# Kernel tuning notes

Hardware: AMD Instinct MI355X
Metric: run time of the kernel (lower is better)

The kernel has to match this reference:

```python
import jax, jax.numpy as jnp
import numpy as np

NL = 2    # num_layers
H = 4     # attention heads
C = 512   # hidden_dim
IN = 256  # in_dim
F = 16    # fanout
B = 256   # seed nodes
NC = 47   # num_classes
DH = C // H
EPS = 1e-5


def _ln(x, g, b):
    mu = jnp.mean(x, -1, keepdims=True)
    var = jnp.mean((x - mu) ** 2, -1, keepdims=True)
    return (x - mu) * jax.lax.rsqrt(var + EPS) * g + b


def _mha(x, wqkv, bqkv, wo, bo):
    # torch nn.MultiheadAttention with a single batch of N tokens
    n = x.shape[0]
    qkv = x @ wqkv.T + bqkv                      # [N, 3C]
    q, k, v = jnp.split(qkv, 3, axis=-1)
    q = q.reshape(n, H, DH).transpose(1, 0, 2)   # [H, N, DH]
    k = k.reshape(n, H, DH).transpose(1, 0, 2)
    v = v.reshape(n, H, DH).transpose(1, 0, 2)
    s = jnp.einsum('hnd,hmd->hnm', q, k) * (1.0 / float(np.sqrt(DH)))
    a = jax.nn.softmax(s, axis=-1)
    o = jnp.einsum('hnm,hmd->hnd', a, v).transpose(1, 0, 2).reshape(n, C)
    return o @ wo.T + bo


def setup_inputs() -> dict:
    ks = jax.random.split(jax.random.key(0), 16)
    n = [B, B * F, B * F * F]
    p = lambda i, shape: jax.random.normal(ks[i], shape, jnp.float32) * 0.02
    return {
        'feats0': jax.random.normal(ks[0], (n[0], IN), jnp.float32),
        'feats1': jax.random.normal(ks[1], (n[1], IN), jnp.float32),
        'feats2': jax.random.normal(ks[2], (n[2], IN), jnp.float32),
        'nmask0': jnp.ones((n[0],), jnp.float32),
        'nmask1': jnp.ones((n[1],), jnp.float32),
        'nmask2': jnp.ones((n[2],), jnp.float32),
        'nbmask0': jax.random.randint(ks[3], (n[0], F), 0, 2, jnp.int32),
        'nbmask1': jax.random.randint(ks[4], (n[1], F), 0, 2, jnp.int32),
        'emb_w': p(5, (C, IN)), 'emb_b': jnp.zeros((C,), jnp.float32),
        'sage_w': p(6, (NL, C, 2 * C)), 'sage_b': jnp.zeros((NL, C), jnp.float32),
        'qkv_w': p(7, (NL, 3 * C, C)), 'qkv_b': jnp.zeros((NL, 3 * C), jnp.float32),
        'out_w': p(8, (NL, C, C)), 'out_b': jnp.zeros((NL, C), jnp.float32),
        'n1_g': jnp.ones((NL, C), jnp.float32), 'n1_b': jnp.zeros((NL, C), jnp.float32),
        'n2_g': jnp.ones((NL, C), jnp.float32), 'n2_b': jnp.zeros((NL, C), jnp.float32),
        'ffn_w1': p(9, (NL, 2 * C, C)), 'ffn_b1': jnp.zeros((NL, 2 * C), jnp.float32),
        'ffn_w2': p(10, (NL, C, 2 * C)), 'ffn_b2': jnp.zeros((NL, C), jnp.float32),
        'cls_w': p(11, (NC, C)), 'cls_b': jnp.zeros((NC,), jnp.float32),
    }


def reference(feats0, feats1, feats2, nmask0, nmask1, nmask2, nbmask0, nbmask1,
              emb_w, emb_b, sage_w, sage_b, qkv_w, qkv_b, out_w, out_b,
              n1_g, n1_b, n2_g, n2_b, ffn_w1, ffn_b1, ffn_w2, ffn_b2, cls_w, cls_b):
    nmasks = [nmask0, nmask1, nmask2]
    nbm = [nbmask0.astype(jnp.float32), nbmask1.astype(jnp.float32)]
    # embedding + node-mask gating per depth
    states = [(f @ emb_w.T + emb_b) * m[:, None]
              for f, m in zip([feats0, feats1, feats2], nmasks)]
    for li in range(NL):
        prev = states
        nxt = list(prev)
        for depth in range(NL - li - 1, -1, -1):
            # masked mean aggregation of sampled neighbors: [n_d, F, C] -> [n_d, C]
            child = prev[depth + 1].reshape(-1, F, C)
            m = nbm[depth][:, :, None]
            summed = jnp.sum(child * m, axis=1)
            denom = jnp.clip(jnp.sum(m, axis=1), 1.0)
            agg = summed / denom
            sf = prev[depth]
            # GraphSAGE concat update (no activation, dropout=0)
            h_local = jnp.concatenate([sf, agg], -1) @ sage_w[li].T + sage_b[li]
            h = _ln(sf + h_local, n1_g[li], n1_b[li])
            h = _ln(h + _mha(h, qkv_w[li], qkv_b[li], out_w[li], out_b[li]),
                    n2_g[li], n2_b[li])
            hf = jax.nn.relu(h @ ffn_w1[li].T + ffn_b1[li]) @ ffn_w2[li].T + ffn_b2[li]
            nxt[depth] = (h + hf) * nmasks[depth][:, None]
        states = nxt
    return states[0] @ cls_w.T + cls_b
```

## Files before the change

kernel.cpp:

```cpp
#include <hip/hip_runtime.h>
#include <math.h>


typedef unsigned short bf16_t;
typedef __attribute__((ext_vector_type(8))) short bf16x8_t;
typedef __attribute__((ext_vector_type(4))) float f32x4_t;

__device__ __forceinline__ bf16_t f2bf(float f) {
  union { float f; unsigned u; } v; v.f = f;
  unsigned r = v.u + 0x7FFFu + ((v.u >> 16) & 1u);
  return (bf16_t)(r >> 16);
}
__device__ __forceinline__ float bf2f(bf16_t u) {
  union { unsigned u; float f; } v; v.u = ((unsigned)u) << 16; return v.f;
}
__device__ __forceinline__ unsigned cvtpk(float lo, float hi) {
  unsigned r;
  asm("v_cvt_pk_bf16_f32 %0, %1, %2" : "=v"(r) : "v"(lo), "v"(hi));
  return r;
}
__device__ __forceinline__ void gload16(const void* g, void* l) {
  __builtin_amdgcn_global_load_lds(
      (const __attribute__((address_space(1))) unsigned int*)g,
      (__attribute__((address_space(3))) unsigned int*)l, 16, 0, 0);
}

#define QSCALE (0.08838834764831845f * 1.4426950408889634f)

template <int BM, int BN, int MODE, bool SPLIT>
__global__ __launch_bounds__(256) void mgemm(
    const bf16_t* __restrict__ A, const bf16_t* __restrict__ A2,
    const bf16_t* __restrict__ W, const float* __restrict__ bias,
    const bf16_t* __restrict__ res, const float* __restrict__ rowa,
    const float* __restrict__ rowb, float* __restrict__ Cf,
    bf16_t* __restrict__ Cb, bf16_t* __restrict__ Vt,
    int M, int N, int K) {
  constexpr int FM = BM / 32, FN = BN / 32;
  constexpr int NCH = (BM + BN) / 16;
  constexpr int CPW = NCH / 4;
  __shared__ bf16_t lds[2][(BM + BN) * 32];
  const int t = threadIdx.x;
  const int w = t >> 6, lane = t & 63;
  const int g = lane >> 4, li = lane & 15;
  const int bm = blockIdx.x * BM, bn = blockIdx.y * BN;
  const int wr = (w >> 1) * (BM / 2), wc = (w & 1) * (BN / 2);
  f32x4_t acc[FM][FN] = {};

  auto stage = [&](int buf, int k0) {
#pragma unroll
    for (int c0 = 0; c0 < CPW; ++c0) {
      const int c = w * CPW + c0;
      const int row = c * 16 + (lane >> 2);
      const int gk = k0 + (lane & 3) * 8;
      const bf16_t* src;
      if (row < BM) {
        if (SPLIT) {
          src = (gk < 512) ? (A + (size_t)(bm + row) * 512 + gk)
                           : (A2 + (size_t)(bm + row) * 512 + (gk - 512));
        } else {
          src = A + (size_t)(bm + row) * K + gk;
        }
      } else {
        src = W + (size_t)(bn + row - BM) * K + gk;
      }
      gload16(src, &lds[buf][c * 512]);
    }
  };

  const int nk = K / 32;
  stage(0, 0);
  for (int ks = 0; ks < nk; ++ks) {
    __syncthreads();
    if (ks + 1 < nk) stage((ks + 1) & 1, (ks + 1) * 32);
    const bf16_t* As = &lds[ks & 1][0];
    const bf16_t* Bs = &lds[ks & 1][BM * 32];
    bf16x8_t af[FM], bfr[FN];
#pragma unroll
    for (int i = 0; i < FM; ++i)
      af[i] = *(const bf16x8_t*)(As + (wr + i * 16 + li) * 32 + g * 8);
#pragma unroll
    for (int j = 0; j < FN; ++j)
      bfr[j] = *(const bf16x8_t*)(Bs + (wc + j * 16 + li) * 32 + g * 8);
#pragma unroll
    for (int i = 0; i < FM; ++i)
#pragma unroll
      for (int j = 0; j < FN; ++j)
        acc[i][j] = __builtin_amdgcn_mfma_f32_16x16x32_bf16(
            af[i], bfr[j], acc[i][j], 0, 0, 0);
  }

#pragma unroll
  for (int i = 0; i < FM; ++i) {
    const int mb = bm + wr + i * 16 + g * 4;
#pragma unroll
    for (int j = 0; j < FN; ++j) {
      const int n = bn + wc + j * 16 + li;
      if (MODE == 5) {
        const float bb = bias[n];
        if (n < 512) {
#pragma unroll
          for (int r = 0; r < 4; ++r)
            Cb[(size_t)(mb + r) * 1024 + n] = f2bf((acc[i][j][r] + bb) * QSCALE);
        } else if (n < 1024) {
#pragma unroll
          for (int r = 0; r < 4; ++r)
            Cb[(size_t)(mb + r) * 1024 + n] = f2bf(acc[i][j][r] + bb);
        } else {
          ushort4 o;
          o.x = f2bf(acc[i][j][0] + bb); o.y = f2bf(acc[i][j][1] + bb);
          o.z = f2bf(acc[i][j][2] + bb); o.w = f2bf(acc[i][j][3] + bb);
          *(ushort4*)(Vt + (size_t)(n - 1024) * M + mb) = o;
        }
      } else {
#pragma unroll
        for (int r = 0; r < 4; ++r) {
          const int m = mb + r;
          const float v = acc[i][j][r];
          if (MODE == 0) Cf[(size_t)m * N + n] = v + bias[n];
          if (MODE == 1) Cb[(size_t)m * N + n] = f2bf((v + bias[n]) * rowa[m]);
          if (MODE == 2)
            Cb[(size_t)m * N + n] = f2bf((v + bias[n] * rowa[m]) * rowb[m]);
          if (MODE == 3) Cb[(size_t)m * N + n] = f2bf(fmaxf(v + bias[n], 0.f));
          if (MODE == 4)
            Cb[(size_t)m * N + n] =
                f2bf((v + bias[n] + bf2f(res[(size_t)m * N + n])) * rowa[m]);
        }
      }
    }
  }
}

template <int SPLITS>
__global__ __launch_bounds__(256) void flashT(
    const bf16_t* __restrict__ qk, const bf16_t* __restrict__ vt,
    bf16_t* __restrict__ attno, float* __restrict__ Of,
    float* __restrict__ Ml, int N) {
  __shared__ bf16_t Ks[2][64 * 128];
  __shared__ bf16_t Vs[2][128 * 64];
  __shared__ bf16_t Ps[4][16 * 64];
  const int bid = blockIdx.x;
  const int sp = bid % SPLITS;
  const int h = (bid / SPLITS) & 3;
  const int qb = bid / (4 * SPLITS);
  const int t = threadIdx.x, w = t >> 6, lane = t & 63;
  const int g = lane >> 4, li = lane & 15;
  const int kvbase = sp * (N / SPLITS);
  const int nt = (N / SPLITS) >> 6;

  bf16x8_t qf[4];
  {
    const bf16_t* qrow = qk + (size_t)(qb * 64 + w * 16 + li) * 1024 + h * 128;
#pragma unroll
    for (int ks = 0; ks < 4; ++ks)
      qf[ks] = *(const bf16x8_t*)(qrow + ks * 32 + g * 8);
  }

  int koff[4], voff[2], pwoff[4];
#pragma unroll
  for (int ks = 0; ks < 4; ++ks)
    koff[ks] = li * 256 + (((ks * 4 + g) ^ (li & 7)) << 4);
#pragma unroll
  for (int ks = 0; ks < 2; ++ks)
    voff[ks] = li * 128 + (((ks * 4 + g) ^ (li & 7)) << 4);
#pragma unroll
  for (int mf = 0; mf < 4; ++mf)
    pwoff[mf] = li * 128 + (((mf * 2 + (g >> 1)) ^ (li & 7)) << 4) +
                ((g & 1) << 3);
  char* Pb = (char*)Ps + w * 2048;

  const bf16_t* kp[4];
  const bf16_t* vp[4];
#pragma unroll
  for (int i = 0; i < 4; ++i) {
    const int c = w * 4 + i;
    const int rk = c * 4 + (lane >> 4);
    kp[i] = qk + (size_t)(kvbase + rk) * 1024 + 512 + h * 128 +
            (((lane & 15) ^ (rk & 7)) * 8);
    const int rv = c * 8 + (lane >> 3);
    vp[i] = vt + (size_t)(h * 128 + rv) * N + kvbase +
            (((lane & 7) ^ (rv & 7)) * 8);
  }
  auto stage = [&](int buf) {
#pragma unroll
    for (int i = 0; i < 4; ++i) {
      const int c = w * 4 + i;
      gload16(kp[i], &Ks[buf][c * 512]);
      kp[i] += 64 * 1024;
      gload16(vp[i], &Vs[buf][c * 512]);
      vp[i] += 64;
    }
  };

  f32x4_t acc[8] = {};
  float mrun = -1e30f, lrun = 0.f;
  stage(0);
  for (int tt = 0; tt < nt; ++tt) {
    const int cur = tt & 1;
    __syncthreads();
    if (tt + 1 < nt) stage(cur ^ 1);
    const char* Kb = (const char*)Ks + cur * 16384;
    const char* Vb = (const char*)Vs + cur * 16384;

    f32x4_t sf[4] = {};
    __builtin_amdgcn_s_setprio(1);
#pragma unroll
    for (int ks = 0; ks < 4; ++ks) {
#pragma unroll
      for (int mf = 0; mf < 4; ++mf) {
        const bf16x8_t kf = *(const bf16x8_t*)(Kb + koff[ks] + mf * 4096);
        sf[mf] =
            __builtin_amdgcn_mfma_f32_16x16x32_bf16(kf, qf[ks], sf[mf], 0, 0, 0);
      }
    }
    __builtin_amdgcn_s_setprio(0);

    float tmax = -1e30f;
#pragma unroll
    for (int mf = 0; mf < 4; ++mf)
#pragma unroll
      for (int r = 0; r < 4; ++r) tmax = fmaxf(tmax, sf[mf][r]);
    tmax = fmaxf(tmax, __shfl_xor(tmax, 16));
    tmax = fmaxf(tmax, __shfl_xor(tmax, 32));
    if (!__all(tmax - mrun <= 11.0f)) {
      const float mnew = fmaxf(mrun, tmax);
      const float fsc = exp2f(mrun - mnew);
      mrun = mnew;
      lrun *= fsc;
#pragma unroll
      for (int mf = 0; mf < 8; ++mf) acc[mf] *= fsc;
    }
    float lsum = 0.f;
#pragma unroll
    for (int mf = 0; mf < 4; ++mf)
#pragma unroll
      for (int r = 0; r < 4; ++r) {
        const float p = exp2f(sf[mf][r] - mrun);
        sf[mf][r] = p;
        lsum += p;
      }
    lsum += __shfl_xor(lsum, 16);
    lsum += __shfl_xor(lsum, 32);
    lrun += lsum;

#pragma unroll
    for (int mf = 0; mf < 4; ++mf) {
      uint2 pv;
      pv.x = cvtpk(sf[mf][0], sf[mf][1]);
      pv.y = cvtpk(sf[mf][2], sf[mf][3]);
      *(uint2*)(Pb + pwoff[mf]) = pv;
    }
    __builtin_amdgcn_s_setprio(1);
#pragma unroll
    for (int ks = 0; ks < 2; ++ks) {
      const bf16x8_t pf = *(const bf16x8_t*)(Pb + voff[ks]);
#pragma unroll
      for (int mf = 0; mf < 8; ++mf) {
        const bf16x8_t vf = *(const bf16x8_t*)(Vb + voff[ks] + mf * 2048);
        acc[mf] =
            __builtin_amdgcn_mfma_f32_16x16x32_bf16(vf, pf, acc[mf], 0, 0, 0);
      }
    }
    __builtin_amdgcn_s_setprio(0);
  }

  if (SPLITS == 1) {
    const float invl = 1.f / lrun;
#pragma unroll
    for (int mf = 0; mf < 8; ++mf) {
      ushort4 o;
      o.x = f2bf(acc[mf][0] * invl); o.y = f2bf(acc[mf][1] * invl);
      o.z = f2bf(acc[mf][2] * invl); o.w = f2bf(acc[mf][3] * invl);
      *(ushort4*)(attno + (size_t)(qb * 64 + w * 16 + li) * 512 + h * 128 +
                  mf * 16 + g * 4) = o;
    }
  } else {
    const int q = qb * 64 + w * 16 + li;
#pragma unroll
    for (int mf = 0; mf < 8; ++mf)
      *(f32x4_t*)(Of + ((size_t)sp * N + q) * 512 + h * 128 + mf * 16 + g * 4) =
          acc[mf];
    if (lane < 16) {
      float2 ml; ml.x = mrun; ml.y = lrun;
      *(float2*)(Ml + ((size_t)(sp * 4 + h) * N + q) * 2) = ml;
    }
  }
}

template <int SPLITS>
__global__ __launch_bounds__(256) void merge_attn(
    const float* __restrict__ Of, const float* __restrict__ Ml,
    bf16_t* __restrict__ attno, int N) {
  const int q = blockIdx.x, t = threadIdx.x;
#pragma unroll
  for (int half = 0; half < 2; ++half) {
    const int c = t + half * 256;
    const int h = c >> 7;
    float2 ml[SPLITS];
    float m = -1e30f;
#pragma unroll
    for (int s = 0; s < SPLITS; ++s) {
      ml[s] = ((const float2*)Ml)[(s * 4 + h) * N + q];
      m = fmaxf(m, ml[s].x);
    }
    float num = 0.f, den = 0.f;
#pragma unroll
    for (int s = 0; s < SPLITS; ++s) {
      const float wgt = exp2f(ml[s].x - m);
      num += Of[((size_t)s * N + q) * 512 + c] * wgt;
      den += ml[s].y * wgt;
    }
    attno[(size_t)q * 512 + c] = f2bf(num / den);
  }
}

__global__ __launch_bounds__(256) void add_ln(
    const bf16_t* __restrict__ X, const float* __restrict__ Y,
    const float* __restrict__ gg, const float* __restrict__ bb,
    bf16_t* __restrict__ out) {
  const int row = blockIdx.x, t = threadIdx.x;
  const size_t base = (size_t)row * 512;
  const float x0 = bf2f(X[base + t]) + Y[base + t];
  const float x1 = bf2f(X[base + 256 + t]) + Y[base + 256 + t];
  float s = x0 + x1, ss = x0 * x0 + x1 * x1;
#pragma unroll
  for (int o = 32; o > 0; o >>= 1) {
    s += __shfl_down(s, o);
    ss += __shfl_down(ss, o);
  }
  __shared__ float rs[4], rss[4], sm[2];
  const int wv = t >> 6, ln = t & 63;
  if (ln == 0) { rs[wv] = s; rss[wv] = ss; }
  __syncthreads();
  if (t == 0) {
    const float S = rs[0] + rs[1] + rs[2] + rs[3];
    const float SS = rss[0] + rss[1] + rss[2] + rss[3];
    const float mean = S * (1.f / 512.f);
    sm[0] = mean;
    sm[1] = rsqrtf(SS * (1.f / 512.f) - mean * mean + 1e-5f);
  }
  __syncthreads();
  const float mean = sm[0], rstd = sm[1];
  out[base + t] = f2bf((x0 - mean) * rstd * gg[t] + bb[t]);
  out[base + 256 + t] = f2bf((x1 - mean) * rstd * gg[t + 256] + bb[t + 256]);
}

__global__ __launch_bounds__(256) void agg_feats(
    const float* __restrict__ feats2, const int* __restrict__ nbm,
    const float* __restrict__ nm2, bf16_t* __restrict__ aggF,
    float* __restrict__ sw, float* __restrict__ invd) {
  const int i = blockIdx.x, t = threadIdx.x;
  float acc = 0.f, ws = 0.f, nbs = 0.f;
#pragma unroll
  for (int j = 0; j < 16; ++j) {
    const float nb = (float)nbm[i * 16 + j];
    const float wj = nb * nm2[i * 16 + j];
    acc += wj * feats2[(size_t)(i * 16 + j) * 256 + t];
    ws += wj;
    nbs += nb;
  }
  aggF[(size_t)i * 256 + t] = f2bf(acc);
  if (t == 0) { sw[i] = ws; invd[i] = 1.f / fmaxf(nbs, 1.f); }
}

__global__ __launch_bounds__(256) void agg_state(
    const bf16_t* __restrict__ src, const int* __restrict__ nbm,
    bf16_t* __restrict__ agg) {
  const int i = blockIdx.x, t = threadIdx.x;
  float a0 = 0.f, a1 = 0.f, nbs = 0.f;
#pragma unroll
  for (int j = 0; j < 16; ++j) {
    const float nb = (float)nbm[i * 16 + j];
    const bf16_t* r = src + (size_t)(i * 16 + j) * 512;
    a0 += nb * bf2f(r[t]);
    a1 += nb * bf2f(r[t + 256]);
    nbs += nb;
  }
  const float inv = 1.f / fmaxf(nbs, 1.f);
  agg[(size_t)i * 512 + t] = f2bf(a0 * inv);
  agg[(size_t)i * 512 + 256 + t] = f2bf(a1 * inv);
}

__global__ __launch_bounds__(256) void cvt_all(
    const float* __restrict__ s_emb, const float* __restrict__ s_sage,
    const float* __restrict__ s_qkv, const float* __restrict__ s_out,
    const float* __restrict__ s_f1, const float* __restrict__ s_f2,
    const float* __restrict__ s_ft0, const float* __restrict__ s_ft1,
    bf16_t* __restrict__ d_emb, bf16_t* __restrict__ d_sage,
    bf16_t* __restrict__ d_qkv, bf16_t* __restrict__ d_out,
    bf16_t* __restrict__ d_f1, bf16_t* __restrict__ d_f2,
    bf16_t* __restrict__ d_ft0, bf16_t* __restrict__ d_ft1) {
  int i = blockIdx.x * 256 + threadIdx.x;
  const float* s; bf16_t* d; int base;
  if (i < 32768)        { s = s_emb;  d = d_emb;  base = 0; }
  else if (i < 294912)  { s = s_sage; d = d_sage; base = 32768; }
  else if (i < 688128)  { s = s_qkv;  d = d_qkv;  base = 294912; }
  else if (i < 819200)  { s = s_out;  d = d_out;  base = 688128; }
  else if (i < 1081344) { s = s_f1;   d = d_f1;   base = 819200; }
  else if (i < 1343488) { s = s_f2;   d = d_f2;   base = 1081344; }
  else if (i < 1359872) { s = s_ft0;  d = d_ft0;  base = 1343488; }
  else                  { s = s_ft1;  d = d_ft1;  base = 1359872; }
  i -= base;
  const float4 v = ((const float4*)s)[i];
  ushort4 o;
  o.x = f2bf(v.x); o.y = f2bf(v.y); o.z = f2bf(v.z); o.w = f2bf(v.w);
  ((ushort4*)d)[i] = o;
}

__global__ __launch_bounds__(256) void cls_k(
    const bf16_t* __restrict__ s, const float* __restrict__ wc,
    const float* __restrict__ bc, float* __restrict__ out) {
  __shared__ float srow[512];
  const int m = blockIdx.x, t = threadIdx.x;
  srow[t] = bf2f(s[(size_t)m * 512 + t]);
  srow[t + 256] = bf2f(s[(size_t)m * 512 + 256 + t]);
  __syncthreads();
  if (t < 47) {
    float a = bc[t];
    const float* wr = wc + (size_t)t * 512;
    for (int k = 0; k < 512; ++k) a += srow[k] * wr[k];
    out[(size_t)m * 47 + t] = a;
  }
}

struct LayerW {
  const bf16_t *wsage, *wqkv, *wout, *wf1, *wf2;
  const float *bsage, *bqkv, *bout, *bf1, *bf2;
  const float *n1g, *n1b, *n2g, *n2b;
};
struct Scratch {
  float* tmp;
  bf16_t *h1, *h2, *qkb, *vt, *attno, *f1o;
  float *Of, *Ml;
};

static void run_block(int n, const bf16_t* sf, const bf16_t* agg,
                      const float* nmask, const LayerW& L, const Scratch& S,
                      bf16_t* sout, hipStream_t st) {
  if (n == 4096) {
    mgemm<64, 128, 0, true><<<dim3(64, 4), 256, 0, st>>>(
        sf, agg, L.wsage, L.bsage, nullptr, nullptr, nullptr, S.tmp, nullptr,
        nullptr, n, 512, 1024);
  } else {
    mgemm<64, 64, 0, true><<<dim3(4, 8), 256, 0, st>>>(
        sf, agg, L.wsage, L.bsage, nullptr, nullptr, nullptr, S.tmp, nullptr,
        nullptr, n, 512, 1024);
  }
  add_ln<<<n, 256, 0, st>>>(sf, S.tmp, L.n1g, L.n1b, S.h1);
  if (n == 4096) {
    mgemm<128, 128, 5, false><<<dim3(32, 12), 256, 0, st>>>(
        S.h1, nullptr, L.wqkv, L.bqkv, nullptr, nullptr, nullptr, nullptr,
        S.qkb, S.vt, n, 1536, 512);
    flashT<2><<<(n / 64) * 8, 256, 0, st>>>(S.qkb, S.vt, nullptr, S.Of, S.Ml, n);
    merge_attn<2><<<n, 256, 0, st>>>(S.Of, S.Ml, S.attno, n);
    mgemm<64, 128, 0, false><<<dim3(64, 4), 256, 0, st>>>(
        S.attno, nullptr, L.wout, L.bout, nullptr, nullptr, nullptr, S.tmp,
        nullptr, nullptr, n, 512, 512);
  } else {
    mgemm<64, 64, 5, false><<<dim3(4, 24), 256, 0, st>>>(
        S.h1, nullptr, L.wqkv, L.bqkv, nullptr, nullptr, nullptr, nullptr,
        S.qkb, S.vt, n, 1536, 512);
    flashT<1><<<(n / 64) * 4, 256, 0, st>>>(S.qkb, S.vt, S.attno, nullptr,
                                            nullptr, n);
    mgemm<64, 64, 0, false><<<dim3(4, 8), 256, 0, st>>>(
        S.attno, nullptr, L.wout, L.bout, nullptr, nullptr, nullptr, S.tmp,
        nullptr, nullptr, n, 512, 512);
  }
  add_ln<<<n, 256, 0, st>>>(S.h1, S.tmp, L.n2g, L.n2b, S.h2);
  if (n == 4096) {
    mgemm<128, 128, 3, false><<<dim3(32, 8), 256, 0, st>>>(
        S.h2, nullptr, L.wf1, L.bf1, nullptr, nullptr, nullptr, nullptr, S.f1o,
        nullptr, n, 1024, 512);
    mgemm<64, 128, 4, false><<<dim3(64, 4), 256, 0, st>>>(
        S.f1o, nullptr, L.wf2, L.bf2, S.h2, nmask, nullptr, nullptr, sout,
        nullptr, n, 512, 1024);
  } else {
    mgemm<64, 64, 3, false><<<dim3(4, 16), 256, 0, st>>>(
        S.h2, nullptr, L.wf1, L.bf1, nullptr, nullptr, nullptr, nullptr, S.f1o,
        nullptr, n, 1024, 512);
    mgemm<64, 64, 4, false><<<dim3(4, 8), 256, 0, st>>>(
        S.f1o, nullptr, L.wf2, L.bf2, S.h2, nmask, nullptr, nullptr, sout,
        nullptr, n, 512, 1024);
  }
}

extern "C" void kernel_launch(void* const* d_in, const int* in_sizes, int n_in,
                              void* d_out, int out_size, void* d_ws,
                              size_t ws_size, hipStream_t stream) {
  const float* feats0 = (const float*)d_in[0];
  const float* feats1 = (const float*)d_in[1];
  const float* feats2 = (const float*)d_in[2];
  const float* nmask0 = (const float*)d_in[3];
  const float* nmask1 = (const float*)d_in[4];
  const float* nmask2 = (const float*)d_in[5];
  const int* nbmask0 = (const int*)d_in[6];
  const int* nbmask1 = (const int*)d_in[7];
  const float* emb_w = (const float*)d_in[8];
  const float* emb_b = (const float*)d_in[9];
  const float* sage_w = (const float*)d_in[10];
  const float* sage_b = (const float*)d_in[11];
  const float* qkv_w = (const float*)d_in[12];
  const float* qkv_b = (const float*)d_in[13];
  const float* out_w = (const float*)d_in[14];
  const float* out_b = (const float*)d_in[15];
  const float* n1_g = (const float*)d_in[16];
  const float* n1_b = (const float*)d_in[17];
  const float* n2_g = (const float*)d_in[18];
  const float* n2_b = (const float*)d_in[19];
  const float* ffn_w1 = (const float*)d_in[20];
  const float* ffn_b1 = (const float*)d_in[21];
  const float* ffn_w2 = (const float*)d_in[22];
  const float* ffn_b2 = (const float*)d_in[23];
  const float* cls_w = (const float*)d_in[24];
  const float* cls_b = (const float*)d_in[25];
  float* out = (float*)d_out;

  size_t off = 0;
  auto alloc = [&](size_t bytes) {
    void* r = (char*)d_ws + off;
    off += (bytes + 255) & ~(size_t)255;
    return r;
  };
  bf16_t* wemb = (bf16_t*)alloc((size_t)512 * 256 * 2);
  bf16_t* wsage = (bf16_t*)alloc((size_t)2 * 512 * 1024 * 2);
  bf16_t* wqkv = (bf16_t*)alloc((size_t)2 * 1536 * 512 * 2);
  bf16_t* wout = (bf16_t*)alloc((size_t)2 * 512 * 512 * 2);
  bf16_t* wf1 = (bf16_t*)alloc((size_t)2 * 1024 * 512 * 2);
  bf16_t* wf2 = (bf16_t*)alloc((size_t)2 * 512 * 1024 * 2);
  bf16_t* f0b = (bf16_t*)alloc((size_t)256 * 256 * 2);
  bf16_t* f1b = (bf16_t*)alloc((size_t)4096 * 256 * 2);
  bf16_t* s0 = (bf16_t*)alloc((size_t)256 * 512 * 2);
  bf16_t* s0b = (bf16_t*)alloc((size_t)256 * 512 * 2);
  bf16_t* s0f = (bf16_t*)alloc((size_t)256 * 512 * 2);
  bf16_t* s1 = (bf16_t*)alloc((size_t)4096 * 512 * 2);
  bf16_t* s1b = (bf16_t*)alloc((size_t)4096 * 512 * 2);
  bf16_t* aggFb = (bf16_t*)alloc((size_t)4096 * 256 * 2);
  float* swv = (float*)alloc((size_t)4096 * 4);
  float* invd = (float*)alloc((size_t)4096 * 4);
  bf16_t* aggb = (bf16_t*)alloc((size_t)4096 * 512 * 2);
  float* tmp = (float*)alloc((size_t)4096 * 512 * 4);
  bf16_t* h1 = (bf16_t*)alloc((size_t)4096 * 512 * 2);
  bf16_t* h2 = (bf16_t*)alloc((size_t)4096 * 512 * 2);
  bf16_t* qkb = (bf16_t*)alloc((size_t)4096 * 1024 * 2);
  bf16_t* vt = (bf16_t*)alloc((size_t)512 * 4096 * 2);
  bf16_t* attno = (bf16_t*)alloc((size_t)4096 * 512 * 2);
  bf16_t* f1o = (bf16_t*)alloc((size_t)4096 * 1024 * 2);
  float* Of = (float*)alloc((size_t)2 * 4096 * 512 * 4);
  float* Ml = (float*)alloc((size_t)2 * 4 * 4096 * 2 * 4);

  cvt_all<<<6336, 256, 0, stream>>>(emb_w, sage_w, qkv_w, out_w, ffn_w1,
                                    ffn_w2, feats0, feats1, wemb, wsage, wqkv,
                                    wout, wf1, wf2, f0b, f1b);

  mgemm<64, 128, 1, false><<<dim3(64, 4), 256, 0, stream>>>(
      f1b, nullptr, wemb, emb_b, nullptr, nmask1, nullptr, nullptr, s1, nullptr,
      4096, 512, 256);
  mgemm<64, 64, 1, false><<<dim3(4, 8), 256, 0, stream>>>(
      f0b, nullptr, wemb, emb_b, nullptr, nmask0, nullptr, nullptr, s0, nullptr,
      256, 512, 256);
  agg_feats<<<4096, 256, 0, stream>>>(feats2, nbmask1, nmask2, aggFb, swv, invd);
  mgemm<64, 128, 2, false><<<dim3(64, 4), 256, 0, stream>>>(
      aggFb, nullptr, wemb, emb_b, nullptr, swv, invd, nullptr, aggb, nullptr,
      4096, 512, 256);

  LayerW L0{wsage, wqkv, wout, wf1, wf2,
            sage_b, qkv_b, out_b, ffn_b1, ffn_b2,
            n1_g, n1_b, n2_g, n2_b};
  LayerW L1{wsage + 512 * 1024, wqkv + 1536 * 512, wout + 512 * 512,
            wf1 + 1024 * 512, wf2 + 512 * 1024,
            sage_b + 512, qkv_b + 1536, out_b + 512, ffn_b1 + 1024,
            ffn_b2 + 512, n1_g + 512, n1_b + 512, n2_g + 512, n2_b + 512};
  Scratch S{tmp, h1, h2, qkb, vt, attno, f1o, Of, Ml};

  run_block(4096, s1, aggb, nmask1, L0, S, s1b, stream);
  agg_state<<<256, 256, 0, stream>>>(s1, nbmask0, aggb);
  run_block(256, s0, aggb, nmask0, L0, S, s0b, stream);
  agg_state<<<256, 256, 0, stream>>>(s1b, nbmask0, aggb);
  run_block(256, s0b, aggb, nmask0, L1, S, s0f, stream);

  cls_k<<<256, 256, 0, stream>>>(s0f, cls_w, cls_b, out);
}
```

Measured before the change: 321.3 us.

## Use 128-row flash tiles with 4 KV splits and bf16 intermediates

The N=4096 attention now runs 128 query rows per block with 512 threads, which halves the K/V reloads per query. The KV sequence is split four ways to keep the grid large. Split partial outputs are normalized and stored as bf16 instead of fp32, and the merge reweights them using l*exp2(m). The GEMM MODE 0 output (the tmp buffer feeding add_ln) also becomes bf16, which cuts memory traffic. In exchange, rounding of intermediates to bf16 adds precision loss, and the extra split adds merge reads.

```diff
diff --git a/kernel.cpp b/kernel.cpp
--- a/kernel.cpp
+++ b/kernel.cpp
@@ -32,7 +32,7 @@
     const bf16_t* __restrict__ A, const bf16_t* __restrict__ A2,
     const bf16_t* __restrict__ W, const float* __restrict__ bias,
     const bf16_t* __restrict__ res, const float* __restrict__ rowa,
-    const float* __restrict__ rowb, float* __restrict__ Cf,
+    const float* __restrict__ rowb,
     bf16_t* __restrict__ Cb, bf16_t* __restrict__ Vt,
     int M, int N, int K) {
   constexpr int FM = BM / 32, FN = BN / 32;
@@ -116,7 +116,7 @@
         for (int r = 0; r < 4; ++r) {
           const int m = mb + r;
           const float v = acc[i][j][r];
-          if (MODE == 0) Cf[(size_t)m * N + n] = v + bias[n];
+          if (MODE == 0) Cb[(size_t)m * N + n] = f2bf(v + bias[n]);
           if (MODE == 1) Cb[(size_t)m * N + n] = f2bf((v + bias[n]) * rowa[m]);
           if (MODE == 2)
             Cb[(size_t)m * N + n] = f2bf((v + bias[n] * rowa[m]) * rowb[m]);
@@ -130,14 +130,16 @@
   }
 }
 
-template <int SPLITS>
-__global__ __launch_bounds__(256) void flashT(
+template <int QB, int SPLITS>
+__global__ __launch_bounds__(QB * 4) void flashT(
     const bf16_t* __restrict__ qk, const bf16_t* __restrict__ vt,
-    bf16_t* __restrict__ attno, float* __restrict__ Of,
+    bf16_t* __restrict__ attno, bf16_t* __restrict__ Ofb,
     float* __restrict__ Ml, int N) {
+  constexpr int NW = QB / 16;
+  constexpr int KCH = 16 / NW;
   __shared__ bf16_t Ks[2][64 * 128];
   __shared__ bf16_t Vs[2][128 * 64];
-  __shared__ bf16_t Ps[4][16 * 64];
+  __shared__ bf16_t Ps[NW][16 * 64];
   const int bid = blockIdx.x;
   const int sp = bid % SPLITS;
   const int h = (bid / SPLITS) & 3;
@@ -149,7 +151,7 @@
 
   bf16x8_t qf[4];
   {
-    const bf16_t* qrow = qk + (size_t)(qb * 64 + w * 16 + li) * 1024 + h * 128;
+    const bf16_t* qrow = qk + (size_t)(qb * QB + w * 16 + li) * 1024 + h * 128;
 #pragma unroll
     for (int ks = 0; ks < 4; ++ks)
       qf[ks] = *(const bf16x8_t*)(qrow + ks * 32 + g * 8);
@@ -168,11 +170,11 @@
                 ((g & 1) << 3);
   char* Pb = (char*)Ps + w * 2048;
 
-  const bf16_t* kp[4];
-  const bf16_t* vp[4];
-#pragma unroll
-  for (int i = 0; i < 4; ++i) {
-    const int c = w * 4 + i;
+  const bf16_t* kp[KCH];
+  const bf16_t* vp[KCH];
+#pragma unroll
+  for (int i = 0; i < KCH; ++i) {
+    const int c = w * KCH + i;
     const int rk = c * 4 + (lane >> 4);
     kp[i] = qk + (size_t)(kvbase + rk) * 1024 + 512 + h * 128 +
             (((lane & 15) ^ (rk & 7)) * 8);
@@ -182,8 +184,8 @@
   }
   auto stage = [&](int buf) {
 #pragma unroll
-    for (int i = 0; i < 4; ++i) {
-      const int c = w * 4 + i;
+    for (int i = 0; i < KCH; ++i) {
+      const int c = w * KCH + i;
       gload16(kp[i], &Ks[buf][c * 512]);
       kp[i] += 64 * 1024;
       gload16(vp[i], &Vs[buf][c * 512]);
@@ -263,22 +265,25 @@
     __builtin_amdgcn_s_setprio(0);
   }
 
+  const float invl = 1.f / lrun;
+  const int q = qb * QB + w * 16 + li;
   if (SPLITS == 1) {
-    const float invl = 1.f / lrun;
 #pragma unroll
     for (int mf = 0; mf < 8; ++mf) {
       ushort4 o;
       o.x = f2bf(acc[mf][0] * invl); o.y = f2bf(acc[mf][1] * invl);
       o.z = f2bf(acc[mf][2] * invl); o.w = f2bf(acc[mf][3] * invl);
-      *(ushort4*)(attno + (size_t)(qb * 64 + w * 16 + li) * 512 + h * 128 +
-                  mf * 16 + g * 4) = o;
+      *(ushort4*)(attno + (size_t)q * 512 + h * 128 + mf * 16 + g * 4) = o;
     }
   } else {
-    const int q = qb * 64 + w * 16 + li;
-#pragma unroll
-    for (int mf = 0; mf < 8; ++mf)
-      *(f32x4_t*)(Of + ((size_t)sp * N + q) * 512 + h * 128 + mf * 16 + g * 4) =
-          acc[mf];
+#pragma unroll
+    for (int mf = 0; mf < 8; ++mf) {
+      ushort4 o;
+      o.x = f2bf(acc[mf][0] * invl); o.y = f2bf(acc[mf][1] * invl);
+      o.z = f2bf(acc[mf][2] * invl); o.w = f2bf(acc[mf][3] * invl);
+      *(ushort4*)(Ofb + ((size_t)sp * N + q) * 512 + h * 128 + mf * 16 +
+                  g * 4) = o;
+    }
     if (lane < 16) {
       float2 ml; ml.x = mrun; ml.y = lrun;
       *(float2*)(Ml + ((size_t)(sp * 4 + h) * N + q) * 2) = ml;
@@ -288,7 +293,7 @@
 
 template <int SPLITS>
 __global__ __launch_bounds__(256) void merge_attn(
-    const float* __restrict__ Of, const float* __restrict__ Ml,
+    const bf16_t* __restrict__ Ofb, const float* __restrict__ Ml,
     bf16_t* __restrict__ attno, int N) {
   const int q = blockIdx.x, t = threadIdx.x;
 #pragma unroll
@@ -305,22 +310,22 @@
     float num = 0.f, den = 0.f;
 #pragma unroll
     for (int s = 0; s < SPLITS; ++s) {
-      const float wgt = exp2f(ml[s].x - m);
-      num += Of[((size_t)s * N + q) * 512 + c] * wgt;
-      den += ml[s].y * wgt;
+      const float wgt = ml[s].y * exp2f(ml[s].x - m);
+      num += bf2f(Ofb[((size_t)s * N + q) * 512 + c]) * wgt;
+      den += wgt;
     }
     attno[(size_t)q * 512 + c] = f2bf(num / den);
   }
 }
 
 __global__ __launch_bounds__(256) void add_ln(
-    const bf16_t* __restrict__ X, const float* __restrict__ Y,
+    const bf16_t* __restrict__ X, const bf16_t* __restrict__ Y,
     const float* __restrict__ gg, const float* __restrict__ bb,
     bf16_t* __restrict__ out) {
   const int row = blockIdx.x, t = threadIdx.x;
   const size_t base = (size_t)row * 512;
-  const float x0 = bf2f(X[base + t]) + Y[base + t];
-  const float x1 = bf2f(X[base + 256 + t]) + Y[base + 256 + t];
+  const float x0 = bf2f(X[base + t]) + bf2f(Y[base + t]);
+  const float x1 = bf2f(X[base + 256 + t]) + bf2f(Y[base + 256 + t]);
   float s = x0 + x1, ss = x0 * x0 + x1 * x1;
 #pragma unroll
   for (int o = 32; o > 0; o >>= 1) {
@@ -428,9 +433,8 @@
   const float *n1g, *n1b, *n2g, *n2b;
 };
 struct Scratch {
-  float* tmp;
-  bf16_t *h1, *h2, *qkb, *vt, *attno, *f1o;
-  float *Of, *Ml;
+  bf16_t *tmpb, *h1, *h2, *qkb, *vt, *attno, *f1o, *Ofb;
+  float *Ml;
 };
 
 static void run_block(int n, const bf16_t* sf, const bf16_t* agg,
@@ -438,48 +442,49 @@
                       bf16_t* sout, hipStream_t st) {
   if (n == 4096) {
     mgemm<64, 128, 0, true><<<dim3(64, 4), 256, 0, st>>>(
-        sf, agg, L.wsage, L.bsage, nullptr, nullptr, nullptr, S.tmp, nullptr,
-        nullptr, n, 512, 1024);
+        sf, agg, L.wsage, L.bsage, nullptr, nullptr, nullptr, S.tmpb, nullptr,
+        n, 512, 1024);
   } else {
     mgemm<64, 64, 0, true><<<dim3(4, 8), 256, 0, st>>>(
-        sf, agg, L.wsage, L.bsage, nullptr, nullptr, nullptr, S.tmp, nullptr,
-        nullptr, n, 512, 1024);
-  }
-  add_ln<<<n, 256, 0, st>>>(sf, S.tmp, L.n1g, L.n1b, S.h1);
+        sf, agg, L.wsage, L.bsage, nullptr, nullptr, nullptr, S.tmpb, nullptr,
+        n, 512, 1024);
+  }
+  add_ln<<<n, 256, 0, st>>>(sf, S.tmpb, L.n1g, L.n1b, S.h1);
   if (n == 4096) {
     mgemm<128, 128, 5, false><<<dim3(32, 12), 256, 0, st>>>(
-        S.h1, nullptr, L.wqkv, L.bqkv, nullptr, nullptr, nullptr, nullptr,
+        S.h1, nullptr, L.wqkv, L.bqkv, nullptr, nullptr, nullptr,
         S.qkb, S.vt, n, 1536, 512);
-    flashT<2><<<(n / 64) * 8, 256, 0, st>>>(S.qkb, S.vt, nullptr, S.Of, S.Ml, n);
-    merge_attn<2><<<n, 256, 0, st>>>(S.Of, S.Ml, S.attno, n);
+    flashT<128, 4><<<(n / 128) * 16, 512, 0, st>>>(S.qkb, S.vt, nullptr, S.Ofb,
+                                                   S.Ml, n);
+    merge_attn<4><<<n, 256, 0, st>>>(S.Ofb, S.Ml, S.attno, n);
     mgemm<64, 128, 0, false><<<dim3(64, 4), 256, 0, st>>>(
-        S.attno, nullptr, L.wout, L.bout, nullptr, nullptr, nullptr, S.tmp,
-        nullptr, nullptr, n, 512, 512);
+        S.attno, nullptr, L.wout, L.bout, nullptr, nullptr, nullptr, S.tmpb,
+        nullptr, n, 512, 512);
   } else {
     mgemm<64, 64, 5, false><<<dim3(4, 24), 256, 0, st>>>(
-        S.h1, nullptr, L.wqkv, L.bqkv, nullptr, nullptr, nullptr, nullptr,
+        S.h1, nullptr, L.wqkv, L.bqkv, nullptr, nullptr, nullptr,
         S.qkb, S.vt, n, 1536, 512);
-    flashT<1><<<(n / 64) * 4, 256, 0, st>>>(S.qkb, S.vt, S.attno, nullptr,
-                                            nullptr, n);
+    flashT<64, 1><<<(n / 64) * 4, 256, 0, st>>>(S.qkb, S.vt, S.attno, nullptr,
+                                                nullptr, n);
     mgemm<64, 64, 0, false><<<dim3(4, 8), 256, 0, st>>>(
-        S.attno, nullptr, L.wout, L.bout, nullptr, nullptr, nullptr, S.tmp,
-        nullptr, nullptr, n, 512, 512);
-  }
-  add_ln<<<n, 256, 0, st>>>(S.h1, S.tmp, L.n2g, L.n2b, S.h2);
+        S.attno, nullptr, L.wout, L.bout, nullptr, nullptr, nullptr, S.tmpb,
+        nullptr, n, 512, 512);
+  }
+  add_ln<<<n, 256, 0, st>>>(S.h1, S.tmpb, L.n2g, L.n2b, S.h2);
   if (n == 4096) {
     mgemm<128, 128, 3, false><<<dim3(32, 8), 256, 0, st>>>(
-        S.h2, nullptr, L.wf1, L.bf1, nullptr, nullptr, nullptr, nullptr, S.f1o,
-        nullptr, n, 1024, 512);
+        S.h2, nullptr, L.wf1, L.bf1, nullptr, nullptr, nullptr, S.f1o, nullptr,
+        n, 1024, 512);
     mgemm<64, 128, 4, false><<<dim3(64, 4), 256, 0, st>>>(
-        S.f1o, nullptr, L.wf2, L.bf2, S.h2, nmask, nullptr, nullptr, sout,
-        nullptr, n, 512, 1024);
+        S.f1o, nullptr, L.wf2, L.bf2, S.h2, nmask, nullptr, sout, nullptr,
+        n, 512, 1024);
   } else {
     mgemm<64, 64, 3, false><<<dim3(4, 16), 256, 0, st>>>(
-        S.h2, nullptr, L.wf1, L.bf1, nullptr, nullptr, nullptr, nullptr, S.f1o,
-        nullptr, n, 1024, 512);
+        S.h2, nullptr, L.wf1, L.bf1, nullptr, nullptr, nullptr, S.f1o, nullptr,
+        n, 1024, 512);
     mgemm<64, 64, 4, false><<<dim3(4, 8), 256, 0, st>>>(
-        S.f1o, nullptr, L.wf2, L.bf2, S.h2, nmask, nullptr, nullptr, sout,
-        nullptr, n, 512, 1024);
+        S.f1o, nullptr, L.wf2, L.bf2, S.h2, nmask, nullptr, sout, nullptr,
+        n, 512, 1024);
   }
 }
 
@@ -537,29 +542,29 @@
   float* swv = (float*)alloc((size_t)4096 * 4);
   float* invd = (float*)alloc((size_t)4096 * 4);
   bf16_t* aggb = (bf16_t*)alloc((size_t)4096 * 512 * 2);
-  float* tmp = (float*)alloc((size_t)4096 * 512 * 4);
+  bf16_t* tmpb = (bf16_t*)alloc((size_t)4096 * 512 * 2);
   bf16_t* h1 = (bf16_t*)alloc((size_t)4096 * 512 * 2);
   bf16_t* h2 = (bf16_t*)alloc((size_t)4096 * 512 * 2);
   bf16_t* qkb = (bf16_t*)alloc((size_t)4096 * 1024 * 2);
   bf16_t* vt = (bf16_t*)alloc((size_t)512 * 4096 * 2);
   bf16_t* attno = (bf16_t*)alloc((size_t)4096 * 512 * 2);
   bf16_t* f1o = (bf16_t*)alloc((size_t)4096 * 1024 * 2);
-  float* Of = (float*)alloc((size_t)2 * 4096 * 512 * 4);
-  float* Ml = (float*)alloc((size_t)2 * 4 * 4096 * 2 * 4);
+  bf16_t* Ofb = (bf16_t*)alloc((size_t)4 * 4096 * 512 * 2);
+  float* Ml = (float*)alloc((size_t)4 * 4 * 4096 * 2 * 4);
 
   cvt_all<<<6336, 256, 0, stream>>>(emb_w, sage_w, qkv_w, out_w, ffn_w1,
                                     ffn_w2, feats0, feats1, wemb, wsage, wqkv,
                                     wout, wf1, wf2, f0b, f1b);
 
   mgemm<64, 128, 1, false><<<dim3(64, 4), 256, 0, stream>>>(
-      f1b, nullptr, wemb, emb_b, nullptr, nmask1, nullptr, nullptr, s1, nullptr,
+      f1b, nullptr, wemb, emb_b, nullptr, nmask1, nullptr, s1, nullptr,
       4096, 512, 256);
   mgemm<64, 64, 1, false><<<dim3(4, 8), 256, 0, stream>>>(
-      f0b, nullptr, wemb, emb_b, nullptr, nmask0, nullptr, nullptr, s0, nullptr,
+      f0b, nullptr, wemb, emb_b, nullptr, nmask0, nullptr, s0, nullptr,
       256, 512, 256);
   agg_feats<<<4096, 256, 0, stream>>>(feats2, nbmask1, nmask2, aggFb, swv, invd);
   mgemm<64, 128, 2, false><<<dim3(64, 4), 256, 0, stream>>>(
-      aggFb, nullptr, wemb, emb_b, nullptr, swv, invd, nullptr, aggb, nullptr,
+      aggFb, nullptr, wemb, emb_b, nullptr, swv, invd, aggb, nullptr,
       4096, 512, 256);
 
   LayerW L0{wsage, wqkv, wout, wf1, wf2,
@@ -569,7 +574,7 @@
             wf1 + 1024 * 512, wf2 + 512 * 1024,
             sage_b + 512, qkv_b + 1536, out_b + 512, ffn_b1 + 1024,
             ffn_b2 + 512, n1_g + 512, n1_b + 512, n2_g + 512, n2_b + 512};
-  Scratch S{tmp, h1, h2, qkb, vt, attno, f1o, Of, Ml};
+  Scratch S{tmpb, h1, h2, qkb, vt, attno, f1o, Ofb, Ml};
 
   run_block(4096, s1, aggb, nmask1, L0, S, s1b, stream);
   agg_state<<<256, 256, 0, stream>>>(s1, nbmask0, aggb);
```

Result: faster. 311.4 us (-3.1%).
